# Kernel optimization log

Hardware: AMD Instinct MI355X
Metric: run time of the kernel (lower is better)

The kernel has to match this reference:

```python
import jax, jax.numpy as jnp
import numpy as np

L = 8          # curve control points per chunk (self.l)
TS = 256       # curve spatial resolution (self.ts)


def setup_inputs() -> dict:
    key = jax.random.key(0)
    k1, k2 = jax.random.split(key)
    # full-resolution input image, values in [0,1)
    x = jax.random.uniform(k1, (4, 3, 1024, 1024), dtype=jnp.float32)
    # predicted curve parameters: 9*L = 72 channels at TS x TS
    param = jax.random.normal(k2, (4, 72, TS, TS), dtype=jnp.float32)
    return {"x": x, "param": param}


def _grid_sample_3d(vol, gx, gy, gz):
    """F.grid_sample(vol, grid, 'bilinear', 'border', align_corners=True)
    vol: [B,C,D,Hc,Wc]; gx,gy,gz: [B,H,W] normalized coords in [-1,1].
    Returns [B,H,W,C] (channels last)."""
    B, C, D, Hc, Wc = vol.shape
    # align_corners=True unnormalization + border padding (clamp coords)
    ix = jnp.clip((gx + 1.0) * 0.5 * (Wc - 1), 0.0, Wc - 1)
    iy = jnp.clip((gy + 1.0) * 0.5 * (Hc - 1), 0.0, Hc - 1)
    iz = jnp.clip((gz + 1.0) * 0.5 * (D - 1), 0.0, D - 1)
    x0f, y0f, z0f = jnp.floor(ix), jnp.floor(iy), jnp.floor(iz)
    wx, wy, wz = ix - x0f, iy - y0f, iz - z0f
    x0 = x0f.astype(jnp.int32); x1 = jnp.minimum(x0 + 1, Wc - 1)
    y0 = y0f.astype(jnp.int32); y1 = jnp.minimum(y0 + 1, Hc - 1)
    z0 = z0f.astype(jnp.int32); z1 = jnp.minimum(z0 + 1, D - 1)
    vol_t = vol.transpose(0, 2, 3, 4, 1)  # [B,D,Hc,Wc,C]
    b = jnp.arange(B)[:, None, None]      # [B,1,1]
    out = jnp.zeros(gx.shape + (C,), dtype=vol.dtype)
    for zi, wz_ in ((z0, 1.0 - wz), (z1, wz)):
        for yi, wy_ in ((y0, 1.0 - wy), (y1, wy)):
            for xi, wx_ in ((x0, 1.0 - wx), (x1, wx)):
                w = (wz_ * wy_ * wx_)[..., None]          # [B,H,W,1]
                out = out + w * vol_t[b, zi, yi, xi]      # gather -> [B,H,W,C]
    return out


def reference(x, param):
    # eval-mode forward of Generator.mapping + tanh (param precomputed by CNN)
    B, _, H, W = x.shape
    Hc, Wc = param.shape[-2], param.shape[-1]
    # torch.stack(torch.chunk(param,3,dim=1),dim=1) == reshape [B,3,3L,Hc,Wc]
    curve = param.reshape(B, 3, 3 * L, Hc, Wc)
    coordh = jnp.linspace(-1.0, 1.0, H, dtype=x.dtype)[:, None]  # varies over H
    coordw = jnp.linspace(-1.0, 1.0, W, dtype=x.dtype)[None, :]  # varies over W
    gx = jnp.broadcast_to(coordw, (B, H, W))
    gy = jnp.broadcast_to(coordh, (B, H, W))
    out = jnp.zeros((B, H, W, 3), dtype=x.dtype)
    for i in range(3):  # three curve chunks, z-coordinate = i-th color channel
        curve_i = curve[:, :, i * L:(i + 1) * L]          # [B,3,L,Hc,Wc]
        out = out + _grid_sample_3d(curve_i, gx, gy, x[:, i])
    return jnp.tanh(out.transpose(0, 3, 1, 2))            # [B,3,H,W]
```

## Files before the change

### kernel.cpp

```cpp
#include <hip/hip_runtime.h>
#include <math.h>

#define IMG 1024
#define HW (IMG * IMG)
#define TS 256
#define CH_STRIDE (TS * TS)
#define PARAM_B_STRIDE (72 * CH_STRIDE)
#define S_CONST (255.0f / 1023.0f)

#define TILE_W 64
#define TILE_H 4
#define ROWS 3
#define CELLS 18
#define CELL_F4 25
#define ROW_F4S (CELLS * CELL_F4)

__global__ __launch_bounds__(256) void curve3d_fused(
    const float* __restrict__ x, const float* __restrict__ param,
    float* __restrict__ out)
{
    __shared__ float4 sh[ROWS * ROW_F4S];
    float* shf = (float*)sh;

    int blk = blockIdx.x;
    int wt = blk & 15;
    int ht = (blk >> 4) & 255;
    int b  = blk >> 12;
    int tid = threadIdx.x;

    int w0 = wt * TILE_W, h0 = ht * TILE_H;
    int xb = (int)((float)w0 * S_CONST);
    int yb = (int)((float)h0 * S_CONST);

    if (tid < 216) {
        int q  = tid / 18;
        int xx = tid - q * 18;
        int xs = min(xb + xx, 255);
        const float* pb = param + (size_t)b * PARAM_B_STRIDE + xs;
        const float* p0 = pb + min(yb + 0, 255) * TS;
        const float* p1 = pb + min(yb + 1, 255) * TS;
        const float* p2 = pb + min(yb + 2, 255) * TS;
        float* d = shf + xx * 100;
#pragma unroll
        for (int rep = 0; rep < 6; ++rep) {
            int ch = q + 12 * rep;
            int z  = ch & 7;
            int m  = ch >> 3;
            int cc = (m * 11) >> 5;
            int ii = m - cc * 3;
            int off = ((ii << 3) + z) * 4 + cc;
            size_t go = (size_t)ch * CH_STRIDE;
            d[off]          = p0[go];
            d[1800 + off]   = p1[go];
            d[3600 + off]   = p2[go];
        }
    }
    __syncthreads();

    int tw = tid & 63, th = tid >> 6;
    int w = w0 + tw, h = h0 + th;

    float ix = (float)w * S_CONST; int x0 = (int)ix; float wx = ix - (float)x0;
    float iy = (float)h * S_CONST; int y0 = (int)iy; float wy = iy - (float)y0;
    int c0 = x0 - xb;
    int c1 = min(x0 + 1, 255) - xb;
    int r0 = y0 - yb;
    int r1 = min(y0 + 1, 255) - yb;

    const float* xp = x + (size_t)b * 3 * HW + (size_t)h * IMG + w;
    int zi[3]; float wz[3];
#pragma unroll
    for (int i = 0; i < 3; ++i) {
        float xv = xp[(size_t)i * HW];
        float izf = fminf(fmaxf(fmaf(xv, 3.5f, 3.5f), 0.0f), 7.0f);
        int z = min((int)izf, 6);
        zi[i] = z;
        wz[i] = izf - (float)z;
    }

    float u0 = 1.0f - wx, v0 = 1.0f - wy;
    float wcs[4] = {v0 * u0, v0 * wx, wy * u0, wy * wx};
    const float4* cell[4] = {
        sh + r0 * ROW_F4S + c0 * CELL_F4,
        sh + r0 * ROW_F4S + c1 * CELL_F4,
        sh + r1 * ROW_F4S + c0 * CELL_F4,
        sh + r1 * ROW_F4S + c1 * CELL_F4
    };

    float acc0 = 0.0f, acc1 = 0.0f, acc2 = 0.0f;
#pragma unroll
    for (int i = 0; i < 3; ++i) {
        int o = (i << 3) + zi[i];
        float wzi = wz[i];
#pragma unroll
        for (int k = 0; k < 4; ++k) {
            float4 a = cell[k][o];
            float4 bv = cell[k][o + 1];
            float wb = wcs[k] * wzi;
            float wa = wcs[k] - wb;
            acc0 = fmaf(a.x, wa, fmaf(bv.x, wb, acc0));
            acc1 = fmaf(a.y, wa, fmaf(bv.y, wb, acc1));
            acc2 = fmaf(a.z, wa, fmaf(bv.z, wb, acc2));
        }
    }

    float* op = out + (size_t)b * 3 * HW + (size_t)h * IMG + w;
    float e0 = __expf(2.0f * acc0);
    float e1 = __expf(2.0f * acc1);
    float e2 = __expf(2.0f * acc2);
    op[0]            = 1.0f - 2.0f / (e0 + 1.0f);
    op[(size_t)HW]   = 1.0f - 2.0f / (e1 + 1.0f);
    op[(size_t)2*HW] = 1.0f - 2.0f / (e2 + 1.0f);
}

extern "C" void kernel_launch(void* const* d_in, const int* in_sizes, int n_in,
                              void* d_out, int out_size, void* d_ws, size_t ws_size,
                              hipStream_t stream) {
    const float* x = (const float*)d_in[0];
    const float* param = (const float*)d_in[1];
    float* out = (float*)d_out;
    curve3d_fused<<<dim3(16 * 256 * 4), dim3(256), 0, stream>>>(x, param, out);
}
```

Before: 210.6 us.

## Widen tiles to 256x4 with coalesced param staging and early x loads

Each block now covers a 256x4 pixel tile with 1024 threads, so fewer blocks reload overlapping param cells. The param tile is staged with coalesced row-wise loads, 64 consecutive x positions per wavefront, into a channel-contiguous LDS layout padded to 77 dwords per cell. The x loads are issued before the staging and the z-index math is done before the barrier to overlap latency. The interpolation now reads float2 pairs per output channel. The larger blocks use about 59KB of LDS and limit occupancy, and the float2 reads at odd offsets may be misaligned.

```diff
diff --git a/kernel.cpp b/kernel.cpp
--- a/kernel.cpp
+++ b/kernel.cpp
@@ -8,57 +8,68 @@
 #define PARAM_B_STRIDE (72 * CH_STRIDE)
 #define S_CONST (255.0f / 1023.0f)
 
-#define TILE_W 64
-#define TILE_H 4
 #define ROWS 3
-#define CELLS 18
-#define CELL_F4 25
-#define ROW_F4S (CELLS * CELL_F4)
+#define CELLS 66
+#define CELL_DW 77
+#define ROW_DW (CELLS * CELL_DW)
+#define LDS_DW (ROWS * ROW_DW)
 
-__global__ __launch_bounds__(256) void curve3d_fused(
+__global__ __launch_bounds__(1024, 8) void curve3d_fused(
     const float* __restrict__ x, const float* __restrict__ param,
     float* __restrict__ out)
 {
-    __shared__ float4 sh[ROWS * ROW_F4S];
-    float* shf = (float*)sh;
-
+    __shared__ float sh[LDS_DW];
     int blk = blockIdx.x;
-    int wt = blk & 15;
-    int ht = (blk >> 4) & 255;
-    int b  = blk >> 12;
+    int wt = blk & 3;
+    int ht = (blk >> 2) & 255;
+    int b  = blk >> 10;
     int tid = threadIdx.x;
 
-    int w0 = wt * TILE_W, h0 = ht * TILE_H;
+    int w0 = wt * 256, h0 = ht * 4;
     int xb = (int)((float)w0 * S_CONST);
     int yb = (int)((float)h0 * S_CONST);
 
-    if (tid < 216) {
-        int q  = tid / 18;
-        int xx = tid - q * 18;
-        int xs = min(xb + xx, 255);
-        const float* pb = param + (size_t)b * PARAM_B_STRIDE + xs;
-        const float* p0 = pb + min(yb + 0, 255) * TS;
-        const float* p1 = pb + min(yb + 1, 255) * TS;
-        const float* p2 = pb + min(yb + 2, 255) * TS;
-        float* d = shf + xx * 100;
+    int tw = tid & 255, th = tid >> 8;
+    int w = w0 + tw, h = h0 + th;
+    const float* xp = x + (size_t)b * 3 * HW + (size_t)h * IMG + w;
+    float xv[3];
+    xv[0] = xp[0]; xv[1] = xp[(size_t)HW]; xv[2] = xp[(size_t)2 * HW];
+
+    int g = tid >> 6, u = tid & 63;
+    const float* pb = param + (size_t)b * PARAM_B_STRIDE;
+    int ys0 = min(yb, 255), ys1 = min(yb + 1, 255), ys2 = min(yb + 2, 255);
 #pragma unroll
-        for (int rep = 0; rep < 6; ++rep) {
-            int ch = q + 12 * rep;
-            int z  = ch & 7;
-            int m  = ch >> 3;
-            int cc = (m * 11) >> 5;
-            int ii = m - cc * 3;
-            int off = ((ii << 3) + z) * 4 + cc;
-            size_t go = (size_t)ch * CH_STRIDE;
-            d[off]          = p0[go];
-            d[1800 + off]   = p1[go];
-            d[3600 + off]   = p2[go];
+    for (int j = 0; j < 14; ++j) {
+        int rid = j * 16 + g;
+        if (rid < 216) {
+            int row = (rid >= 144) ? 2 : ((rid >= 72) ? 1 : 0);
+            int ch = rid - row * 72;
+            int ys = (row == 2) ? ys2 : ((row == 1) ? ys1 : ys0);
+            float v = pb[(size_t)ch * CH_STRIDE + ys * TS + (xb + u)];
+            sh[row * ROW_DW + u * CELL_DW + ch] = v;
         }
     }
+    if (tid < 432) {
+        int rid = tid >> 1;
+        int xx = 64 + (tid & 1);
+        int row = (rid >= 144) ? 2 : ((rid >= 72) ? 1 : 0);
+        int ch = rid - row * 72;
+        int ys = (row == 2) ? ys2 : ((row == 1) ? ys1 : ys0);
+        int xs = min(xb + xx, 255);
+        sh[row * ROW_DW + xx * CELL_DW + ch] =
+            pb[(size_t)ch * CH_STRIDE + ys * TS + xs];
+    }
+
+    int zi[3]; float wz[3];
+#pragma unroll
+    for (int i = 0; i < 3; ++i) {
+        float izf = fminf(fmaxf(fmaf(xv[i], 3.5f, 3.5f), 0.0f), 7.0f);
+        int z = min((int)izf, 6);
+        zi[i] = z;
+        wz[i] = izf - (float)z;
+    }
+
     __syncthreads();
-
-    int tw = tid & 63, th = tid >> 6;
-    int w = w0 + tw, h = h0 + th;
 
     float ix = (float)w * S_CONST; int x0 = (int)ix; float wx = ix - (float)x0;
     float iy = (float)h * S_CONST; int y0 = (int)iy; float wy = iy - (float)y0;
@@ -67,50 +78,35 @@
     int r0 = y0 - yb;
     int r1 = min(y0 + 1, 255) - yb;
 
-    const float* xp = x + (size_t)b * 3 * HW + (size_t)h * IMG + w;
-    int zi[3]; float wz[3];
-#pragma unroll
-    for (int i = 0; i < 3; ++i) {
-        float xv = xp[(size_t)i * HW];
-        float izf = fminf(fmaxf(fmaf(xv, 3.5f, 3.5f), 0.0f), 7.0f);
-        int z = min((int)izf, 6);
-        zi[i] = z;
-        wz[i] = izf - (float)z;
-    }
-
     float u0 = 1.0f - wx, v0 = 1.0f - wy;
     float wcs[4] = {v0 * u0, v0 * wx, wy * u0, wy * wx};
-    const float4* cell[4] = {
-        sh + r0 * ROW_F4S + c0 * CELL_F4,
-        sh + r0 * ROW_F4S + c1 * CELL_F4,
-        sh + r1 * ROW_F4S + c0 * CELL_F4,
-        sh + r1 * ROW_F4S + c1 * CELL_F4
+    const float* bases[4] = {
+        sh + r0 * ROW_DW + c0 * CELL_DW,
+        sh + r0 * ROW_DW + c1 * CELL_DW,
+        sh + r1 * ROW_DW + c0 * CELL_DW,
+        sh + r1 * ROW_DW + c1 * CELL_DW
     };
 
-    float acc0 = 0.0f, acc1 = 0.0f, acc2 = 0.0f;
+    float* op = out + (size_t)b * 3 * HW + (size_t)h * IMG + w;
 #pragma unroll
-    for (int i = 0; i < 3; ++i) {
-        int o = (i << 3) + zi[i];
-        float wzi = wz[i];
+    for (int c = 0; c < 3; ++c) {
+        float acc = 0.0f;
 #pragma unroll
-        for (int k = 0; k < 4; ++k) {
-            float4 a = cell[k][o];
-            float4 bv = cell[k][o + 1];
-            float wb = wcs[k] * wzi;
-            float wa = wcs[k] - wb;
-            acc0 = fmaf(a.x, wa, fmaf(bv.x, wb, acc0));
-            acc1 = fmaf(a.y, wa, fmaf(bv.y, wb, acc1));
-            acc2 = fmaf(a.z, wa, fmaf(bv.z, wb, acc2));
+        for (int i = 0; i < 3; ++i) {
+            int off = (c * 3 + i) * 8 + zi[i];
+            float wzi = wz[i];
+#pragma unroll
+            for (int k = 0; k < 4; ++k) {
+                float2 v;
+                __builtin_memcpy(&v, bases[k] + off, 8);
+                float wb = wcs[k] * wzi;
+                float wa = wcs[k] - wb;
+                acc = fmaf(v.x, wa, fmaf(v.y, wb, acc));
+            }
         }
+        float e = __expf(2.0f * acc);
+        op[(size_t)c * HW] = 1.0f - 2.0f / (e + 1.0f);
     }
-
-    float* op = out + (size_t)b * 3 * HW + (size_t)h * IMG + w;
-    float e0 = __expf(2.0f * acc0);
-    float e1 = __expf(2.0f * acc1);
-    float e2 = __expf(2.0f * acc2);
-    op[0]            = 1.0f - 2.0f / (e0 + 1.0f);
-    op[(size_t)HW]   = 1.0f - 2.0f / (e1 + 1.0f);
-    op[(size_t)2*HW] = 1.0f - 2.0f / (e2 + 1.0f);
 }
 
 extern "C" void kernel_launch(void* const* d_in, const int* in_sizes, int n_in,
@@ -119,5 +115,5 @@
     const float* x = (const float*)d_in[0];
     const float* param = (const float*)d_in[1];
     float* out = (float*)d_out;
-    curve3d_fused<<<dim3(16 * 256 * 4), dim3(256), 0, stream>>>(x, param, out);
+    curve3d_fused<<<dim3(4 * 256 * 4), dim3(1024), 0, stream>>>(x, param, out);
 }
```

New measurement: 185.1 us. -12.1%, faster.
